# Optimization experiments

Measured on AMD Instinct MI355X. Metric: run time of the kernel, lower is better.

## Reference

```python
import jax, jax.numpy as jnp
import numpy as np


def setup_inputs() -> dict:
    key = jax.random.key(0)
    k_x, k_q, k_k, k_v = jax.random.split(key, 4)
    B, S, E, D = 4, 2048, 1024, 1024
    scale = 1.0 / np.sqrt(E)
    return {
        "x": jax.random.normal(k_x, (B, S, E), dtype=jnp.float32),
        # nn.Linear weight matrices, shape [out_dim, in_dim]; y = x @ W.T
        "w_q": jax.random.normal(k_q, (D, E), dtype=jnp.float32) * scale,
        "w_k": jax.random.normal(k_k, (D, E), dtype=jnp.float32) * scale,
        "w_v": jax.random.normal(k_v, (D, E), dtype=jnp.float32) * scale,
    }


def reference(x, w_q, w_k, w_v):
    # x: [B, S, E]; w_*: [D, E] (torch nn.Linear convention)
    B, S, E = x.shape
    q = jnp.einsum("bse,de->bsd", x, w_q)  # [B, S, D]
    k = jnp.einsum("bse,de->bsd", x, w_k)
    v = jnp.einsum("bse,de->bsd", x, w_v)
    D = q.shape[-1]
    # raw scores, then causal mask (strictly upper triangle -> -inf), then
    # scale by 1/sqrt(D) inside softmax exactly as the original does.
    scores = jnp.einsum("bsd,btd->bst", q, k)  # [B, S, S]
    causal = jnp.tril(jnp.ones((S, S), dtype=bool))  # True = keep
    scores = jnp.where(causal[None], scores, -jnp.inf)
    attn = jax.nn.softmax(scores / jnp.sqrt(jnp.asarray(D, x.dtype)), axis=-1)
    # dropout p=0.0 -> identity
    return jnp.einsum("bst,btd->bsd", attn, v)  # [B, S, D]
```

## Files before the change

kernel.cpp:

```cpp
#include <hip/hip_runtime.h>
#include <hip/hip_bf16.h>


typedef unsigned short u16;
typedef __attribute__((ext_vector_type(4))) u16   u16x4;
typedef __attribute__((ext_vector_type(8))) u16   u16x8;
typedef __attribute__((ext_vector_type(8))) short short8;
typedef __attribute__((ext_vector_type(4))) float f32x4;
typedef __attribute__((ext_vector_type(4))) int   i32x4;

__device__ inline u16 f2b(float v) {
    __hip_bfloat16 b = __float2bfloat16(v);
    return *reinterpret_cast<u16*>(&b);
}
__device__ inline float b2f(u16 v) {
    unsigned int u = ((unsigned int)v) << 16;
    return *reinterpret_cast<float*>(&u);
}

template <typename T> __device__ inline void store_elem(T* p, float v);
template <> __device__ inline void store_elem<float>(float* p, float v) { *p = v; }
template <> __device__ inline void store_elem<u16>(u16* p, float v)     { *p = f2b(v); }

__device__ inline void gload_lds16(const u16* g, u16* l) {
    __builtin_amdgcn_global_load_lds(
        (const __attribute__((address_space(1))) void*)g,
        (__attribute__((address_space(3))) void*)l, 16, 0, 0);
}

__global__ __launch_bounds__(256) void cast_all_kernel(
    const float* __restrict__ x,  const float* __restrict__ wq,
    const float* __restrict__ wk, const float* __restrict__ wv,
    u16* __restrict__ dst) {
    int q = blockIdx.x * 256 + threadIdx.x;
    const float* src;
    int sidx;
    if (q < 2097152) { src = x; sidx = q * 4; }
    else {
        int qq = q - 2097152;
        int w  = qq >> 18;
        sidx   = (qq & 262143) * 4;
        src    = (w == 0) ? wq : (w == 1) ? wk : wv;
    }
    float4 v = *(const float4*)(src + sidx);
    u16x4 o;
    o.x = f2b(v.x); o.y = f2b(v.y); o.z = f2b(v.z); o.w = f2b(v.w);
    *(u16x4*)(dst + q * 4) = o;
}

#define MT 128
#define NT 128
#define BKH 32
#define HSZ (MT * BKH)

template <int TRANS, typename OutT>
__device__ __forceinline__ void gemm_core(
    u16* __restrict__ As, u16* __restrict__ Bs,
    const u16* __restrict__ Ab, int lda,
    const u16* __restrict__ Bb, int ldb,
    OutT* __restrict__ Cb, int ldc,
    int m0, int n0, int kbeg, int kend)
{
    const int tid  = threadIdx.x;
    const int lane = tid & 63;
    const int wave = tid >> 6;
    const int quad = lane >> 4;
    const int r16  = lane & 15;
    const int mw   = (wave >> 1) * 64;
    const int nw   = (wave & 1) * 64;

    const int c0 = tid, c1 = tid + 256;
    const int r0 = c0 >> 2, k0 = (c0 & 3) * 8;
    const int r1 = c1 >> 2, k1 = (c1 & 3) * 8;
    const int oa0 = (m0 + r0) * lda + k0;
    const int oa1 = (m0 + r1) * lda + k1;
    const int ob0 = (n0 + r0) * ldb + k0;
    const int ob1 = (n0 + r1) * ldb + k1;

    f32x4 acc[4][4] = {};

    for (int kk = kbeg; kk < kend; kk += 2 * BKH) {
        __syncthreads();
        gload_lds16(Ab + (kk + oa0),        &As[c0 * 8]);
        gload_lds16(Ab + (kk + oa1),        &As[c1 * 8]);
        gload_lds16(Ab + (kk + BKH + oa0),  &As[HSZ + c0 * 8]);
        gload_lds16(Ab + (kk + BKH + oa1),  &As[HSZ + c1 * 8]);
        gload_lds16(Bb + (kk + ob0),        &Bs[c0 * 8]);
        gload_lds16(Bb + (kk + ob1),        &Bs[c1 * 8]);
        gload_lds16(Bb + (kk + BKH + ob0),  &Bs[HSZ + c0 * 8]);
        gload_lds16(Bb + (kk + BKH + ob1),  &Bs[HSZ + c1 * 8]);
        __syncthreads();

#pragma unroll
        for (int h = 0; h < 2; h++) {
            short8 af[4], bf[4];
#pragma unroll
            for (int i = 0; i < 4; i++)
                af[i] = *(const short8*)&As[h * HSZ + (mw + i * 16 + r16) * BKH + quad * 8];
#pragma unroll
            for (int j = 0; j < 4; j++)
                bf[j] = *(const short8*)&Bs[h * HSZ + (nw + j * 16 + r16) * BKH + quad * 8];
#pragma unroll
            for (int i = 0; i < 4; i++)
#pragma unroll
                for (int j = 0; j < 4; j++)
                    acc[i][j] = __builtin_amdgcn_mfma_f32_16x16x32_bf16(af[i], bf[j], acc[i][j], 0, 0, 0);
        }
    }

    if (TRANS == 0) {
#pragma unroll
        for (int i = 0; i < 4; i++)
#pragma unroll
            for (int j = 0; j < 4; j++)
#pragma unroll
                for (int r = 0; r < 4; r++) {
                    int m = m0 + mw + i * 16 + quad * 4 + r;
                    int n = n0 + nw + j * 16 + r16;
                    store_elem(&Cb[(long long)m * ldc + n], acc[i][j][r]);
                }
    } else {
#pragma unroll
        for (int i = 0; i < 4; i++)
#pragma unroll
            for (int j = 0; j < 4; j++) {
                int mbase = m0 + mw + i * 16 + quad * 4;
                int d     = n0 + nw + j * 16 + r16;
                int b     = mbase >> 11;
                int s     = mbase & 2047;
                u16x4 o;
#pragma unroll
                for (int r = 0; r < 4; r++) o[r] = f2b(acc[i][j][r]);
                *(u16x4*)((u16*)Cb + (((b << 10) + d) * 2048 + s)) = o;
            }
    }
}

__global__ __launch_bounds__(256, 4) void gemm_qkv(
    const u16* __restrict__ xb, const u16* __restrict__ wb,
    u16* __restrict__ qk, u16* __restrict__ vt) {
    __shared__ __align__(16) u16 As[2 * HSZ];
    __shared__ __align__(16) u16 Bs[2 * HSZ];
    int bx = blockIdx.x, m0 = blockIdx.y * MT;
    if (bx < 16)
        gemm_core<0, u16>(As, Bs, xb, 1024, wb, 1024, qk, 2048,
                          m0, bx * 128, 0, 1024);
    else
        gemm_core<1, u16>(As, Bs, xb, 1024, wb + 2048 * 1024, 1024, vt, 2048,
                          m0, (bx - 16) * 128, 0, 1024);
}

__global__ __launch_bounds__(256, 4) void gemm_scores(
    const u16* __restrict__ qk, u16* __restrict__ sc) {
    __shared__ __align__(16) u16 As[2 * HSZ];
    __shared__ __align__(16) u16 Bs[2 * HSZ];
    int t = blockIdx.x;
    float ff = sqrtf(8.0f * t + 1.0f);
    int m = (int)((ff - 1.0f) * 0.5f);
    while ((m + 1) * (m + 2) / 2 <= t) m++;
    while (m * (m + 1) / 2 > t) m--;
    int m0 = m * MT;
    int n0 = (t - m * (m + 1) / 2) * NT;
    const u16* Ab = qk + (long long)blockIdx.z * 2048 * 2048;
    const u16* Bb = Ab + 1024;
    u16* Cb = sc + (long long)blockIdx.z * 2048 * 2048;
    gemm_core<0, u16>(As, Bs, Ab, 2048, Bb, 2048, Cb, 2048, m0, n0, 0, 1024);
}

__global__ __launch_bounds__(256, 4) void gemm_pv(
    const u16* __restrict__ P, const u16* __restrict__ vt,
    float* __restrict__ out, float* __restrict__ part)
{
    __shared__ __align__(16) u16 As[2 * HSZ];
    __shared__ __align__(16) u16 Bs[2 * HSZ];
    const int bid = blockIdx.x;
    int m, chunk, n;
    if (bid < 80) {
        int q = bid >> 3; n = bid & 7;
        if (q < 9) { m = 7 + q; chunk = 0; } else { m = 15; chunk = 1; }
    } else {
        int r = bid - 80; int s = 7 - (r >> 4); int t = r & 15;
        n = t & 7;
        if (t < 8) { m = s - 1; chunk = 0; } else { m = s + 7; chunk = 1; }
    }
    const int m0 = m * MT, n0 = n * NT;
    const int kbeg = chunk ? 1024 : 0;
    const int kend = chunk ? (m0 + MT) : min(1024, m0 + MT);
    const int b = blockIdx.z;

    const u16* Ab = P  + (long long)b * 2048 * 2048;
    const u16* Bb = vt + (long long)b * 1024 * 2048;
    float* Cb = (chunk == 0)
        ? out  + (long long)b * 2097152
        : part + (long long)b * 1048576 - 1024LL * 1024;
    gemm_core<0, float>(As, Bs, Ab, 2048, Bb, 2048, Cb, 1024, m0, n0, kbeg, kend);
}

__global__ __launch_bounds__(256) void pv_combine(float* __restrict__ out,
                                                  const float* __restrict__ part) {
    long long idx = ((long long)blockIdx.x * 256 + threadIdx.x) * 8;
    long long bb = idx >> 20;
    long long j  = idx & 1048575;
    float* o = out + bb * 2097152 + 1048576 + j;
    const float* p = part + bb * 1048576 + j;
    float4 o0 = *(float4*)o, o1 = *(float4*)(o + 4);
    float4 p0 = *(const float4*)p, p1 = *(const float4*)(p + 4);
    o0.x += p0.x; o0.y += p0.y; o0.z += p0.z; o0.w += p0.w;
    o1.x += p1.x; o1.y += p1.y; o1.z += p1.z; o1.w += p1.w;
    *(float4*)o = o0; *(float4*)(o + 4) = o1;
}

__global__ __launch_bounds__(256) void softmax_kernel(const u16* __restrict__ sc,
                                                      u16* __restrict__ P) {
    const int S = 2048;
    int row = blockIdx.x;
    int i   = row & (S - 1);
    int n   = i + 1;
    int kendr = (i & ~127) + 128;
    const u16* srow = sc + (long long)row * S;
    u16*       prow = P  + (long long)row * S;

    int j0 = threadIdx.x * 8;
    u16x8 raw = {};
    if (j0 <= i) raw = *(const u16x8*)(srow + j0);
    float v[8];
#pragma unroll
    for (int e = 0; e < 8; e++) v[e] = (j0 + e < n) ? b2f(raw[e]) : -1e30f;

    __shared__ float red[8];
    float lmax = v[0];
#pragma unroll
    for (int e = 1; e < 8; e++) lmax = fmaxf(lmax, v[e]);
    for (int o = 32; o > 0; o >>= 1) lmax = fmaxf(lmax, __shfl_xor(lmax, o, 64));
    int wid = threadIdx.x >> 6;
    if ((threadIdx.x & 63) == 0) red[wid] = lmax;
    __syncthreads();
    float Mx = fmaxf(fmaxf(red[0], red[1]), fmaxf(red[2], red[3]));

    const float C = 0.045112384f;
    float ev[8];
    float lsum = 0.f;
#pragma unroll
    for (int e = 0; e < 8; e++) {
        ev[e] = (j0 + e < n) ? exp2f((v[e] - Mx) * C) : 0.f;
        lsum += ev[e];
    }
    for (int o = 32; o > 0; o >>= 1) lsum += __shfl_xor(lsum, o, 64);
    if ((threadIdx.x & 63) == 0) red[4 + wid] = lsum;
    __syncthreads();
    float inv = 1.0f / (red[4] + red[5] + red[6] + red[7]);

    if (j0 < kendr) {
        u16x8 o8;
#pragma unroll
        for (int e = 0; e < 8; e++) o8[e] = f2b(ev[e] * inv);
        *(u16x8*)(prow + j0) = o8;
    }
}

extern "C" void kernel_launch(void* const* d_in, const int* in_sizes, int n_in,
                              void* d_out, int out_size, void* d_ws, size_t ws_size,
                              hipStream_t stream) {
    const float* x  = (const float*)d_in[0];
    const float* wq = (const float*)d_in[1];
    const float* wk = (const float*)d_in[2];
    const float* wv = (const float*)d_in[3];
    float* out = (float*)d_out;

    char* ws = (char*)d_ws;
    u16*   xb   = (u16*)(ws);
    u16*   wb   = (u16*)(ws + 16777216LL);
    u16*   qk   = (u16*)(ws + 23068672LL);
    u16*   sc   = (u16*)(ws + 56623104LL);
    u16*   P    = (u16*)(ws + 90177536LL);
    u16*   vt   = (u16*)(ws + 123731968LL);
    float* part = (float*)(ws + 140509184LL);

    cast_all_kernel<<<11264, 256, 0, stream>>>(x, wq, wk, wv, xb);

    gemm_qkv<<<dim3(24, 64, 1), 256, 0, stream>>>(xb, wb, qk, vt);

    gemm_scores<<<dim3(136, 1, 4), 256, 0, stream>>>(qk, sc);

    softmax_kernel<<<8192, 256, 0, stream>>>(sc, P);

    gemm_pv<<<dim3(192, 1, 4), 256, 0, stream>>>(P, vt, out, part);
    pv_combine<<<2048, 256, 0, stream>>>(out, part);
}
```

Baseline: 243.8 us.

## Split-K the scores GEMM and use atomic accumulation in PV instead of combine

The scores GEMM is split in half along K (doubling the grid), and each half writes its own bf16 partial score buffer, which softmax then sums. The PV GEMM drops the separate partial buffer and combine kernel: rows in the lower half are zeroed with memsets and both K-chunks accumulate into the output with float atomics. This aims to improve occupancy of the triangular scores launch and remove one kernel launch plus its extra traffic. In exchange it adds a second score buffer write and read, four memsets, atomic contention, and rounding error from summing two bf16 partial scores.

```diff
diff --git a/kernel.cpp b/kernel.cpp
--- a/kernel.cpp
+++ b/kernel.cpp
@@ -108,7 +108,7 @@
         }
     }
 
-    if (TRANS == 0) {
+    if (TRANS == 0 || TRANS == 2) {
 #pragma unroll
         for (int i = 0; i < 4; i++)
 #pragma unroll
@@ -117,7 +117,11 @@
                 for (int r = 0; r < 4; r++) {
                     int m = m0 + mw + i * 16 + quad * 4 + r;
                     int n = n0 + nw + j * 16 + r16;
-                    store_elem(&Cb[(long long)m * ldc + n], acc[i][j][r]);
+                    if (TRANS == 0)
+                        store_elem(&Cb[(long long)m * ldc + n], acc[i][j][r]);
+                    else
+                        unsafeAtomicAdd((float*)&Cb[(long long)m * ldc + n],
+                                        acc[i][j][r]);
                 }
     } else {
 #pragma unroll
@@ -151,10 +155,11 @@
 }
 
 __global__ __launch_bounds__(256, 4) void gemm_scores(
-    const u16* __restrict__ qk, u16* __restrict__ sc) {
+    const u16* __restrict__ qk, u16* __restrict__ sc0, u16* __restrict__ sc1) {
     __shared__ __align__(16) u16 As[2 * HSZ];
     __shared__ __align__(16) u16 Bs[2 * HSZ];
-    int t = blockIdx.x;
+    int bx = blockIdx.x;
+    int t = bx >> 1, half = bx & 1;
     float ff = sqrtf(8.0f * t + 1.0f);
     int m = (int)((ff - 1.0f) * 0.5f);
     while ((m + 1) * (m + 2) / 2 <= t) m++;
@@ -163,13 +168,14 @@
     int n0 = (t - m * (m + 1) / 2) * NT;
     const u16* Ab = qk + (long long)blockIdx.z * 2048 * 2048;
     const u16* Bb = Ab + 1024;
-    u16* Cb = sc + (long long)blockIdx.z * 2048 * 2048;
-    gemm_core<0, u16>(As, Bs, Ab, 2048, Bb, 2048, Cb, 2048, m0, n0, 0, 1024);
+    u16* Cb = (half ? sc1 : sc0) + (long long)blockIdx.z * 2048 * 2048;
+    gemm_core<0, u16>(As, Bs, Ab, 2048, Bb, 2048, Cb, 2048,
+                      m0, n0, half * 512, half * 512 + 512);
 }
 
 __global__ __launch_bounds__(256, 4) void gemm_pv(
     const u16* __restrict__ P, const u16* __restrict__ vt,
-    float* __restrict__ out, float* __restrict__ part)
+    float* __restrict__ out)
 {
     __shared__ __align__(16) u16 As[2 * HSZ];
     __shared__ __align__(16) u16 Bs[2 * HSZ];
@@ -190,42 +196,37 @@
 
     const u16* Ab = P  + (long long)b * 2048 * 2048;
     const u16* Bb = vt + (long long)b * 1024 * 2048;
-    float* Cb = (chunk == 0)
-        ? out  + (long long)b * 2097152
-        : part + (long long)b * 1048576 - 1024LL * 1024;
-    gemm_core<0, float>(As, Bs, Ab, 2048, Bb, 2048, Cb, 1024, m0, n0, kbeg, kend);
-}
-
-__global__ __launch_bounds__(256) void pv_combine(float* __restrict__ out,
-                                                  const float* __restrict__ part) {
-    long long idx = ((long long)blockIdx.x * 256 + threadIdx.x) * 8;
-    long long bb = idx >> 20;
-    long long j  = idx & 1048575;
-    float* o = out + bb * 2097152 + 1048576 + j;
-    const float* p = part + bb * 1048576 + j;
-    float4 o0 = *(float4*)o, o1 = *(float4*)(o + 4);
-    float4 p0 = *(const float4*)p, p1 = *(const float4*)(p + 4);
-    o0.x += p0.x; o0.y += p0.y; o0.z += p0.z; o0.w += p0.w;
-    o1.x += p1.x; o1.y += p1.y; o1.z += p1.z; o1.w += p1.w;
-    *(float4*)o = o0; *(float4*)(o + 4) = o1;
-}
-
-__global__ __launch_bounds__(256) void softmax_kernel(const u16* __restrict__ sc,
+    float* Cb = out + (long long)b * 2097152;
+    if (m < 8)
+        gemm_core<0, float>(As, Bs, Ab, 2048, Bb, 2048, Cb, 1024,
+                            m0, n0, kbeg, kend);
+    else
+        gemm_core<2, float>(As, Bs, Ab, 2048, Bb, 2048, Cb, 1024,
+                            m0, n0, kbeg, kend);
+}
+
+__global__ __launch_bounds__(256) void softmax_kernel(const u16* __restrict__ sc0,
+                                                      const u16* __restrict__ sc1,
                                                       u16* __restrict__ P) {
     const int S = 2048;
     int row = blockIdx.x;
     int i   = row & (S - 1);
     int n   = i + 1;
     int kendr = (i & ~127) + 128;
-    const u16* srow = sc + (long long)row * S;
-    u16*       prow = P  + (long long)row * S;
+    const u16* s0row = sc0 + (long long)row * S;
+    const u16* s1row = sc1 + (long long)row * S;
+    u16*       prow  = P   + (long long)row * S;
 
     int j0 = threadIdx.x * 8;
-    u16x8 raw = {};
-    if (j0 <= i) raw = *(const u16x8*)(srow + j0);
+    u16x8 raw0 = {}, raw1 = {};
+    if (j0 <= i) {
+        raw0 = *(const u16x8*)(s0row + j0);
+        raw1 = *(const u16x8*)(s1row + j0);
+    }
     float v[8];
 #pragma unroll
-    for (int e = 0; e < 8; e++) v[e] = (j0 + e < n) ? b2f(raw[e]) : -1e30f;
+    for (int e = 0; e < 8; e++)
+        v[e] = (j0 + e < n) ? b2f(raw0[e]) + b2f(raw1[e]) : -1e30f;
 
     __shared__ float red[8];
     float lmax = v[0];
@@ -268,22 +269,25 @@
     float* out = (float*)d_out;
 
     char* ws = (char*)d_ws;
-    u16*   xb   = (u16*)(ws);
-    u16*   wb   = (u16*)(ws + 16777216LL);
-    u16*   qk   = (u16*)(ws + 23068672LL);
-    u16*   sc   = (u16*)(ws + 56623104LL);
-    u16*   P    = (u16*)(ws + 90177536LL);
-    u16*   vt   = (u16*)(ws + 123731968LL);
-    float* part = (float*)(ws + 140509184LL);
+    u16* xb  = (u16*)(ws);
+    u16* wb  = (u16*)(ws + 16777216LL);
+    u16* qk  = (u16*)(ws + 23068672LL);
+    u16* sc0 = (u16*)(ws + 56623104LL);
+    u16* sc1 = (u16*)(ws + 90177536LL);
+    u16* P   = (u16*)(ws + 123731968LL);
+    u16* vt  = (u16*)(ws + 157286400LL);
 
     cast_all_kernel<<<11264, 256, 0, stream>>>(x, wq, wk, wv, xb);
 
+    for (int b = 0; b < 4; b++)
+        hipMemsetAsync(out + (long long)b * 2097152 + 1048576, 0,
+                       4194304, stream);
+
     gemm_qkv<<<dim3(24, 64, 1), 256, 0, stream>>>(xb, wb, qk, vt);
 
-    gemm_scores<<<dim3(136, 1, 4), 256, 0, stream>>>(qk, sc);
-
-    softmax_kernel<<<8192, 256, 0, stream>>>(sc, P);
-
-    gemm_pv<<<dim3(192, 1, 4), 256, 0, stream>>>(P, vt, out, part);
-    pv_combine<<<2048, 256, 0, stream>>>(out, part);
-}
+    gemm_scores<<<dim3(272, 1, 4), 256, 0, stream>>>(qk, sc0, sc1);
+
+    softmax_kernel<<<8192, 256, 0, stream>>>(sc0, sc1, P);
+
+    gemm_pv<<<dim3(192, 1, 4), 256, 0, stream>>>(P, vt, out);
+}
```

Result: no change. 244.2 us (+0.2%).
